# Optimization experiments

Hardware: AMD Instinct MI355X
Metric: run time of the kernel (lower is better)

The kernel has to match this reference:

```python
import jax, jax.numpy as jnp
import numpy as np
from jax import lax

N = 2; C_IN = 256
H0, W0 = 100, 152
H1, W1 = 50, 76
DYN_CH = 34            # 4 init_offset + 4 bound_pt_offset + 18 semantic_pt_offset + 8 reg_aggr_attn
REG_CH = 4             # 4 boundary points x 1 channel each
NUM_CLASSES = 80
SEM_PTS = 9
CLS_CH = SEM_PTS * NUM_CLASSES
BOUND_PTS = 4
RATIO = 0.5            # LIMIT_BOUND_POINT_OFFSET_RATIO

_BASE = np.array([[1,0,0,0],[0,1,0,0],[0.5,0,0.5,0],
                  [0,0.5,0,0.5],[0,0,1,0],[0,0,0,1]], np.float32)
BOUND_MAT = jnp.asarray(_BASE[[0,3,2,1,4,3,2,5]])                      # (8,4) box -> cross-shaped 4 pts
SEM_MAT = jnp.asarray(_BASE[[0,1,0,3,0,5,2,1,2,3,2,5,4,1,4,3,4,5]])    # (18,4) box -> 3x3 pts
BOUND_OFF_IDX = jnp.array([1, 2, 5, 6])   # tangential coordinate channel of each boundary point
LOC_IDX = jnp.array([0, 3, 4, 7])         # box-side coordinate channel of each boundary point

def conv3x3(x, w, b):
    y = lax.conv_general_dilated(x, w, (1, 1), 'SAME',
                                 dimension_numbers=('NCHW', 'OIHW', 'NCHW'))
    return y + b[None, :, None, None]

def conv1x1(x, w):
    return jnp.einsum('oi,nihw->nohw', w[:, :, 0, 0], x)

def pred_collect(fmap, pts, point_num, reduce_points, bias=None):
    # Bilinearly sample per-point channel groups of fmap at dynamic point locations.
    # fmap: (N, P*c, Hm, Wm); pts: (N, 2P, H, W) with (x, y) pairs per point.
    Nb, C, Hm, Wm = fmap.shape
    P = point_num; c = C // P
    H, W = pts.shape[2], pts.shape[3]
    fm = fmap.reshape(Nb, P, c, Hm, Wm)
    pg = pts.reshape(Nb, P, 2, H, W)
    def sample(f, pt):  # f: (c, Hm, Wm), pt: (2, H, W)
        x = jnp.clip(pt[0], 0.0, Wm - 1.0)
        y = jnp.clip(pt[1], 0.0, Hm - 1.0)
        x0 = jnp.floor(x); y0 = jnp.floor(y)
        fx = x - x0; fy = y - y0
        x0i = x0.astype(jnp.int32); y0i = y0.astype(jnp.int32)
        x1i = jnp.minimum(x0i + 1, Wm - 1); y1i = jnp.minimum(y0i + 1, Hm - 1)
        v00 = f[:, y0i, x0i]; v01 = f[:, y0i, x1i]
        v10 = f[:, y1i, x0i]; v11 = f[:, y1i, x1i]
        return v00*(1-fx)*(1-fy) + v01*fx*(1-fy) + v10*(1-fx)*fy + v11*fx*fy
    vals = jax.vmap(jax.vmap(sample))(fm, pg)  # (N, P, c, H, W)
    if reduce_points:
        out = vals.sum(axis=1)
        if bias is not None:
            out = out + bias[None, :, None, None]
        return out
    return vals.reshape(Nb, P * c, H, W)

def head_forward(reg_feats, cls_feats, anchors, dyn_w, dyn_b, reg_w, cls_w, cls_b):
    reg_maps = [conv1x1(x, reg_w) for x in reg_feats]
    cls_maps = [conv1x1(x, cls_w) for x in cls_feats]
    cls_scores, coarse_boxes, reg_boxes = [], [], []
    for i, (reg_feat, anchor) in enumerate(zip(reg_feats, anchors)):
        Nb, _, H, W = reg_feat.shape
        pred = conv3x3(reg_feat, dyn_w, dyn_b)
        init_off, bpt_off, spt_off, attn = jnp.split(pred, [4, 8, 26], axis=1)
        coarse = anchor + init_off                                  # (N,4,H,W) = (x1,y1,x2,y2)
        # straight-through clamp of boundary-point tangential offsets to +-wh/2*ratio
        bpt_off = bpt_off.reshape(Nb, 2, 2, 1, H, W)
        wh = jnp.stack([coarse[:, 3] - coarse[:, 1],
                        coarse[:, 2] - coarse[:, 0]], axis=1) / 2 * RATIO  # (N,2,H,W) [h,w]
        thres = wh[:, None, :, None]                                # (N,1,2,1,H,W)
        extra = jnp.maximum(bpt_off - thres, 0.0) + jnp.minimum(bpt_off + thres, 0.0)
        bpt_off = (bpt_off - lax.stop_gradient(extra)).reshape(Nb, 4, H, W)
        bound_pt = lax.stop_gradient(jnp.einsum('oc,nchw->nohw', BOUND_MAT, coarse))
        bound_pt = bound_pt.at[:, BOUND_OFF_IDX].add(bpt_off)       # (N,8,H,W)
        bound_pt_loc = bound_pt[:, LOC_IDX]                         # (N,4,H,W)
        reg_val = pred_collect(reg_maps[i], bound_pt, BOUND_PTS, False)  # (N,4,H,W)
        if i > 0:
            attn_sm = jax.nn.softmax(attn.reshape(Nb, BOUND_PTS, 2, H, W), axis=2)
            reg_hi = reg_val.reshape(Nb, BOUND_PTS, 1, 1, H, W)
            reg_lo = pred_collect(reg_maps[i - 1], bound_pt * 2, BOUND_PTS, False)
            reg_lo = reg_lo.reshape(Nb, BOUND_PTS, 1, 1, H, W) * 0.5
            reg_val = (jnp.concatenate([reg_lo, reg_hi], axis=2)
                       * attn_sm[:, :, :, None]).sum(axis=2).reshape(Nb, -1, H, W)
        reg_box = (lax.stop_gradient(bound_pt_loc) + reg_val).reshape(Nb, 4, -1, H, W).mean(axis=2)
        sem_pt = lax.stop_gradient(jnp.einsum('oc,nchw->nohw', SEM_MAT, coarse)) + spt_off
        cls_score = pred_collect(cls_maps[i], sem_pt, SEM_PTS, True, cls_b)  # (N,80,H,W)
        cls_scores.append(cls_score); coarse_boxes.append(coarse); reg_boxes.append(reg_box)
    return cls_scores, coarse_boxes, reg_boxes

def make_anchor(H, W):
    gy, gx = jnp.meshgrid(jnp.arange(H, dtype=jnp.float32),
                          jnp.arange(W, dtype=jnp.float32), indexing='ij')
    a = jnp.stack([gx - 4.0, gy - 4.0, gx + 4.0, gy + 4.0], axis=0)
    return jnp.broadcast_to(a[None], (N, 4, H, W))

def setup_inputs() -> dict:
    key = jax.random.key(0)
    ks = jax.random.split(key, 7)
    return {
        "reg_feat0": jax.random.normal(ks[0], (N, C_IN, H0, W0), jnp.float32),
        "reg_feat1": jax.random.normal(ks[1], (N, C_IN, H1, W1), jnp.float32),
        "cls_feat0": jax.random.normal(ks[2], (N, C_IN, H0, W0), jnp.float32),
        "cls_feat1": jax.random.normal(ks[3], (N, C_IN, H1, W1), jnp.float32),
        "anchor0": make_anchor(H0, W0),
        "anchor1": make_anchor(H1, W1),
        "dyn_w": jax.random.normal(ks[4], (DYN_CH, C_IN, 3, 3), jnp.float32) * 0.01,
        "dyn_b": jnp.zeros((DYN_CH,), jnp.float32),
        "reg_w": jax.random.normal(ks[5], (REG_CH, C_IN, 1, 1), jnp.float32) * 0.05,
        "cls_w": jax.random.normal(ks[6], (CLS_CH, C_IN, 1, 1), jnp.float32) * 0.05,
        "cls_b": jnp.zeros((NUM_CLASSES,), jnp.float32),
    }

def reference(reg_feat0, reg_feat1, cls_feat0, cls_feat1, anchor0, anchor1,
              dyn_w, dyn_b, reg_w, cls_w, cls_b):
    cls_scores, coarse_boxes, reg_boxes = head_forward(
        [reg_feat0, reg_feat1], [cls_feat0, cls_feat1], [anchor0, anchor1],
        dyn_w, dyn_b, reg_w, cls_w, cls_b)
    return (*cls_scores, *coarse_boxes, *reg_boxes)
```

## Files before the change

### kernel.cpp

```cpp
#include <hip/hip_runtime.h>
#include <hip/hip_bf16.h>
#include <cstdint>

#define N_BATCH 2
#define C_IN 256
#define DYN_CH 34
#define CLS_CH 720
#define NUM_CLASSES 80
#define NCOMB 48

#define P0c 15200
#define P1c 3800
#define M0c 30400
#define M1c 7600
#define MT0c 119
#define MT1c 30
#define CT0c 475
#define CT1c 119

typedef __attribute__((ext_vector_type(8))) short short8;
typedef __attribute__((ext_vector_type(4))) float f32x4;

typedef const unsigned int __attribute__((address_space(1)))* gas1_t;
typedef unsigned int __attribute__((address_space(3)))* las3_t;

__device__ __forceinline__ void async_ld16(const void* g, void* l) {
  __builtin_amdgcn_global_load_lds((gas1_t)g, (las3_t)l, 16, 0, 0);
}

__global__ __launch_bounds__(256) void pack_feat(
    const float* __restrict__ cls0, const float* __restrict__ cls1,
    const float* __restrict__ reg0, const float* __restrict__ reg1,
    const float* __restrict__ cls_w, const float* __restrict__ dyn_w,
    const float* __restrict__ reg_w, __hip_bfloat16* __restrict__ a0,
    __hip_bfloat16* __restrict__ a1, __hip_bfloat16* __restrict__ r0,
    __hip_bfloat16* __restrict__ r1, __hip_bfloat16* __restrict__ bpack,
    __hip_bfloat16* __restrict__ wpack) {
  int b = blockIdx.x;
  if (b >= 2384) {
    b -= 2384;
    if (b < 90) {
      int u = b * 256 + threadIdx.x;
      if (u >= 9 * 32 * 80) return;
      int ntile = u / 2560;
      int rem = u % 2560;
      int kcg = rem / 80;
      int ochl = rem % 80;
      int och = ntile * 80 + ochl;
      const float* wr = cls_w + (size_t)och * C_IN + kcg * 8;
      __hip_bfloat16 tmp[8];
#pragma unroll
      for (int c = 0; c < 8; ++c) tmp[c] = __float2bfloat16(wr[c]);
      *(uint4*)(bpack + (size_t)u * 8) = *(const uint4*)tmp;
    } else {
      int u = (b - 90) * 256 + threadIdx.x;
      if (u >= 13824) return;
      int j = u / 768;
      int r = u % 768;
      int n = r / 16;
      int s = r % 16;
      int ku = j * 16 + (s ^ (n & 7));
      int k0 = ku * 8;
      int tap = k0 >> 8;
      int c0 = k0 & 255;
      __hip_bfloat16 tmp[8];
#pragma unroll
      for (int i = 0; i < 8; ++i) {
        int c = c0 + i;
        float v = 0.f;
        if (n < DYN_CH) v = dyn_w[((size_t)n * C_IN + c) * 9 + tap];
        else if (n < DYN_CH + 4 && tap == 4)
          v = reg_w[(size_t)(n - DYN_CH) * C_IN + c];
        tmp[i] = __float2bfloat16(v);
      }
      *(uint4*)(wpack + (size_t)u * 8) = *(const uint4*)tmp;
    }
    return;
  }
  int j = b & 7;
  int mtg = b >> 3;
  const float* src;
  __hip_bfloat16* dst;
  int P, Mtot, mtile;
  if (mtg < 119)      { src = cls0; dst = a0; P = P0c; Mtot = M0c; mtile = mtg; }
  else if (mtg < 149) { src = cls1; dst = a1; P = P1c; Mtot = M1c; mtile = mtg - 119; }
  else if (mtg < 268) { src = reg0; dst = r0; P = P0c; Mtot = M0c; mtile = mtg - 149; }
  else                { src = reg1; dst = r1; P = P1c; Mtot = M1c; mtile = mtg - 268; }
  int wave = threadIdx.x >> 6;
  int lane = threadIdx.x & 63;
  int kcg = j * 4 + wave;
  int c0 = kcg * 8;
  int m4 = mtile * 256 + lane * 4;
  uint4* du = (uint4*)dst + (size_t)mtile * 8192 + (size_t)kcg * 256 + lane * 4;
  if (m4 < Mtot) {
    int n = m4 / P;
    int p = m4 - n * P;
    const float* sp = src + ((size_t)n * C_IN + c0) * P + p;
    float4 f[8];
#pragma unroll
    for (int c = 0; c < 8; ++c) f[c] = *(const float4*)(sp + (size_t)c * P);
#pragma unroll
    for (int i = 0; i < 4; ++i) {
      union { uint4 u; __hip_bfloat16 h[8]; } o;
#pragma unroll
      for (int c = 0; c < 8; ++c) {
        float v = (i == 0) ? f[c].x : (i == 1) ? f[c].y : (i == 2) ? f[c].z : f[c].w;
        o.h[c] = __float2bfloat16(v);
      }
      du[i] = o.u;
    }
  } else {
    uint4 z = {0u, 0u, 0u, 0u};
#pragma unroll
    for (int i = 0; i < 4; ++i) du[i] = z;
  }
}

__global__ __launch_bounds__(512) void cls_gemm_mfma(
    const uint4* __restrict__ Ap0, const uint4* __restrict__ Ap1,
    const uint4* __restrict__ Bp, __hip_bfloat16* __restrict__ out0,
    __hip_bfloat16* __restrict__ out1) {
  __shared__ uint4 Bsh[2560];
  int bb = blockIdx.x;
  int g = bb & 7;
  int loc = bb >> 3;
  int lm = loc / 9;
  int ntile = loc - lm * 9;
  int mtile = g * 19 + lm;
  if (mtile >= MT0c + MT1c) return;
  int tid = threadIdx.x;
  int w = tid >> 6;
  int lane = tid & 63;
  int l15 = lane & 15;
  int kq = lane >> 4;

  const uint4* Ap;
  __hip_bfloat16* out;
  int Mtot;
  if (mtile < MT0c) { Ap = Ap0; out = out0; Mtot = M0c; }
  else              { mtile -= MT0c; Ap = Ap1; out = out1; Mtot = M1c; }

  const uint4* Ab = Ap + (size_t)mtile * 8192;
  const uint4* Bb = Bp + (size_t)ntile * 2560;

#pragma unroll
  for (int i = 0; i < 5; ++i)
    async_ld16(Bb + i * 512 + w * 64 + lane, &Bsh[i * 512 + w * 64]);
  __syncthreads();

  f32x4 acc[2][5];
#pragma unroll
  for (int i = 0; i < 2; ++i)
#pragma unroll
    for (int j = 0; j < 5; ++j) acc[i][j] = (f32x4)0.f;

  const uint4* Abase = Ab + kq * 256 + w * 32 + l15;
#pragma unroll 2
  for (int kb = 0; kb < 8; ++kb) {
    uint4 a[2];
#pragma unroll
    for (int mi = 0; mi < 2; ++mi) a[mi] = Abase[kb * 1024 + mi * 16];
    short8 b[5];
    const uint4* Br = &Bsh[kb * 320 + kq * 80 + l15];
#pragma unroll
    for (int ni = 0; ni < 5; ++ni) b[ni] = *(const short8*)&Br[ni * 16];
#pragma unroll
    for (int mi = 0; mi < 2; ++mi)
#pragma unroll
      for (int ni = 0; ni < 5; ++ni)
        acc[mi][ni] = __builtin_amdgcn_mfma_f32_16x16x32_bf16(
            *(const short8*)&a[mi], b[ni], acc[mi][ni], 0, 0, 0);
  }

  int gbase = mtile * 256 + w * 32;
#pragma unroll
  for (int mi = 0; mi < 2; ++mi) {
#pragma unroll
    for (int r = 0; r < 4; ++r) {
      int gg = gbase + mi * 16 + kq * 4 + r;
      if (gg >= Mtot) continue;
      __hip_bfloat16* orow = out + (size_t)gg * CLS_CH + ntile * 80 + l15;
#pragma unroll
      for (int ni = 0; ni < 5; ++ni)
        orow[ni * 16] = __float2bfloat16(acc[mi][ni][r]);
    }
  }
}

__global__ __launch_bounds__(256) void dyn_reg_conv_mfma(
    const uint4* __restrict__ rp0, const uint4* __restrict__ rp1,
    const uint4* __restrict__ wp, float* __restrict__ part0,
    float* __restrict__ part1) {
  __shared__ uint4 Bs[768];
  int g = blockIdx.x & 7;
  int loc = blockIdx.x >> 3;
  int lm = loc / 3;
  int seg = loc - lm * 3;
  int bx = g * 75 + lm;
  if (bx >= CT0c + CT1c) return;
  int tid = threadIdx.x;
  int wave = tid >> 6;
  int lane = tid & 63;
  int l15 = lane & 15;
  int kq = lane >> 4;

  const uint4* rp;
  float* part;
  int Mtot, P, W, H;
  if (bx < CT0c) { rp = rp0; part = part0; Mtot = M0c; P = P0c; W = 152; H = 100; }
  else { bx -= CT0c; rp = rp1; part = part1; Mtot = M1c; P = P1c; W = 76; H = 50; }

  int m = bx * 64 + wave * 16 + l15;
  bool mval = (m < Mtot);
  int mc = mval ? m : 0;
  int n = mc / P;
  int rem = mc - n * P;
  int y = rem / W;
  int x = rem - y * W;

  f32x4 acc[3];
#pragma unroll
  for (int i = 0; i < 3; ++i) acc[i] = (f32x4)0.f;

  for (int jj = 0; jj < 6; ++jj) {
    int j = seg * 6 + jj;
    const uint4* wsrc = wp + (size_t)j * 768 + wave * 192;
#pragma unroll
    for (int i = 0; i < 3; ++i)
      async_ld16(wsrc + i * 64 + lane, &Bs[wave * 192 + i * 64]);

    int tap = j >> 1;
    int cb8 = (j & 1) * 16;
    int dy = tap / 3 - 1, dx = tap % 3 - 1;
    int sy = y + dy, sx = x + dx;
    bool val = mval && ((unsigned)sy < (unsigned)H) && ((unsigned)sx < (unsigned)W);
    int sm = m + dy * W + dx;
    int smc = val ? sm : 0;
    size_t tbase = (size_t)(smc >> 8) * 8192 + (smc & 255);
    uint4 a[4];
#pragma unroll
    for (int t = 0; t < 4; ++t) {
      uint4 v = {0u, 0u, 0u, 0u};
      if (val) v = rp[tbase + (size_t)(cb8 + t * 4 + kq) * 256];
      a[t] = v;
    }
    __syncthreads();
#pragma unroll
    for (int t = 0; t < 4; ++t) {
#pragma unroll
      for (int ni = 0; ni < 3; ++ni) {
        int nn = ni * 16 + l15;
        short8 bf = *(const short8*)&Bs[nn * 16 + ((t * 4 + kq) ^ (nn & 7))];
        acc[ni] = __builtin_amdgcn_mfma_f32_16x16x32_bf16(
            *(short8*)&a[t], bf, acc[ni], 0, 0, 0);
      }
    }
    __syncthreads();
  }

  int mrow = bx * 64 + wave * 16 + kq * 4;
#pragma unroll
  for (int r = 0; r < 4; ++r) {
    int mm = mrow + r;
    if (mm >= Mtot) continue;
    float* dst = part + ((size_t)seg * Mtot + mm) * NCOMB + l15;
#pragma unroll
    for (int ni = 0; ni < 3; ++ni) dst[ni * 16] = acc[ni][r];
  }
}

__device__ __forceinline__ float samp48(const float* __restrict__ part,
                                        int Mtot, int nbase, int W, int H,
                                        float px, float py, int ch) {
  float xc = fminf(fmaxf(px, 0.f), (float)(W - 1));
  float yc = fminf(fmaxf(py, 0.f), (float)(H - 1));
  float x0f = floorf(xc), y0f = floorf(yc);
  float fx = xc - x0f, fy = yc - y0f;
  int x0 = (int)x0f, y0 = (int)y0f;
  int x1 = min(x0 + 1, W - 1), y1 = min(y0 + 1, H - 1);
  size_t m00 = (size_t)(nbase + y0 * W + x0);
  size_t m01 = (size_t)(nbase + y0 * W + x1);
  size_t m10 = (size_t)(nbase + y1 * W + x0);
  size_t m11 = (size_t)(nbase + y1 * W + x1);
  float v00 = 0.f, v01 = 0.f, v10 = 0.f, v11 = 0.f;
#pragma unroll
  for (int s = 0; s < 3; ++s) {
    size_t off = (size_t)s * Mtot;
    v00 += part[(off + m00) * NCOMB + ch];
    v01 += part[(off + m01) * NCOMB + ch];
    v10 += part[(off + m10) * NCOMB + ch];
    v11 += part[(off + m11) * NCOMB + ch];
  }
  return v00 * (1.f - fx) * (1.f - fy) + v01 * fx * (1.f - fy) +
         v10 * (1.f - fx) * fy + v11 * fx * fy;
}

__global__ __launch_bounds__(64) void decode(
    const float* __restrict__ part0, const float* __restrict__ part1,
    const float* __restrict__ dyn_b, const float* __restrict__ anchor0,
    const float* __restrict__ anchor1, float* __restrict__ out_coarse0,
    float* __restrict__ out_coarse1, float* __restrict__ out_regbox0,
    float* __restrict__ out_regbox1, int4* __restrict__ sidx0,
    float4* __restrict__ swt0, int4* __restrict__ sidx1,
    float4* __restrict__ swt1) {
  int g = blockIdx.x & 7;
  int loc = blockIdx.x >> 3;
  int u = g * 75 + loc;
  if (u >= 594) return;
  const float* part;
  const float* anchor;
  float* out_coarse;
  float* out_regbox;
  int4* sidx;
  float4* swt;
  int Mtot, H, W, P, level, m;
  if (u < 475) {
    part = part0; anchor = anchor0; out_coarse = out_coarse0;
    out_regbox = out_regbox0; sidx = sidx0; swt = swt0;
    Mtot = M0c; H = 100; W = 152; P = P0c; level = 0;
    m = u * 64 + threadIdx.x;
  } else {
    part = part1; anchor = anchor1; out_coarse = out_coarse1;
    out_regbox = out_regbox1; sidx = sidx1; swt = swt1;
    Mtot = M1c; H = 50; W = 76; P = P1c; level = 1;
    m = (u - 475) * 64 + threadIdx.x;
  }
  if (m >= Mtot) return;
  int n = m / P;
  int p = m - n * P;
  float pr[40];
  {
    const float4* q0 = (const float4*)(part + (size_t)m * NCOMB);
    const float4* q1 = (const float4*)(part + ((size_t)Mtot + m) * NCOMB);
    const float4* q2 = (const float4*)(part + ((size_t)2 * Mtot + m) * NCOMB);
#pragma unroll
    for (int o4 = 0; o4 < 10; ++o4) {
      float4 a = q0[o4], b = q1[o4], c = q2[o4];
      pr[4 * o4 + 0] = a.x + b.x + c.x;
      pr[4 * o4 + 1] = a.y + b.y + c.y;
      pr[4 * o4 + 2] = a.z + b.z + c.z;
      pr[4 * o4 + 3] = a.w + b.w + c.w;
    }
#pragma unroll
    for (int o = 0; o < DYN_CH; ++o) pr[o] += dyn_b[o];
  }
  const float* an = anchor + (size_t)n * 4 * P + p;
  float cb[4];
#pragma unroll
  for (int k = 0; k < 4; ++k) cb[k] = an[(size_t)k * P] + pr[k];
  float* oc = out_coarse + (size_t)n * 4 * P + p;
#pragma unroll
  for (int k = 0; k < 4; ++k) oc[(size_t)k * P] = cb[k];

  float thr_y = (cb[3] - cb[1]) * 0.25f;
  float thr_x = (cb[2] - cb[0]) * 0.25f;
  float bo[4];
#pragma unroll
  for (int j = 0; j < 4; ++j) {
    float thr = (j & 1) ? thr_x : thr_y;
    float b = pr[4 + j];
    float extra = fmaxf(b - thr, 0.f) + fminf(b + thr, 0.f);
    bo[j] = b - extra;
  }
  float cx = 0.5f * (cb[0] + cb[2]);
  float cy = 0.5f * (cb[1] + cb[3]);
  float bp[8] = {cb[0], cy + bo[0], cx + bo[1], cb[1],
                 cb[2], cy + bo[2], cx + bo[3], cb[3]};

  int nbase = n * P;
  int nbaseLo = n * P0c;
  float rb[4];
#pragma unroll
  for (int pt = 0; pt < 4; ++pt) {
    float hi = samp48(part, Mtot, nbase, W, H, bp[2 * pt], bp[2 * pt + 1],
                      DYN_CH + pt);
    float val;
    if (level == 0) {
      val = hi;
    } else {
      float lo = 0.5f * samp48(part0, M0c, nbaseLo, 152, 100, bp[2 * pt] * 2.f,
                               bp[2 * pt + 1] * 2.f, DYN_CH + pt);
      float e0 = pr[26 + 2 * pt], e1 = pr[26 + 2 * pt + 1];
      float mx = fmaxf(e0, e1);
      float w0 = expf(e0 - mx), w1 = expf(e1 - mx);
      val = (lo * w0 + hi * w1) / (w0 + w1);
    }
    rb[pt] = val;
  }
  float* orb = out_regbox + (size_t)n * 4 * P + p;
  orb[0] = bp[0] + rb[0];
  orb[(size_t)P] = bp[3] + rb[1];
  orb[(size_t)2 * P] = bp[4] + rb[2];
  orb[(size_t)3 * P] = bp[7] + rb[3];

  float sx[9] = {cb[0], cb[0], cb[0], cx, cx, cx, cb[2], cb[2], cb[2]};
  float sy[9] = {cb[1], cy, cb[3], cb[1], cy, cb[3], cb[1], cy, cb[3]};
#pragma unroll
  for (int k = 0; k < 9; ++k) {
    float px = sx[k] + pr[8 + 2 * k];
    float py = sy[k] + pr[8 + 2 * k + 1];
    float xc = fminf(fmaxf(px, 0.f), (float)(W - 1));
    float yc = fminf(fmaxf(py, 0.f), (float)(H - 1));
    float x0f = floorf(xc), y0f = floorf(yc);
    float fx = xc - x0f, fy = yc - y0f;
    int x0 = (int)x0f, y0 = (int)y0f;
    int x1 = min(x0 + 1, W - 1), y1 = min(y0 + 1, H - 1);
    int4 iv;
    iv.x = (nbase + y0 * W + x0) * CLS_CH + k * 80;
    iv.y = (x1 - x0) * CLS_CH;
    iv.z = (y1 - y0) * W * CLS_CH;
    iv.w = 0;
    sidx[(size_t)k * Mtot + m] = iv;
    float4 wv = {(1.f - fx) * (1.f - fy), fx * (1.f - fy), (1.f - fx) * fy,
                 fx * fy};
    swt[(size_t)k * Mtot + m] = wv;
  }
}

__global__ __launch_bounds__(256) void cls_gather_f(
    const __hip_bfloat16* __restrict__ map0,
    const __hip_bfloat16* __restrict__ map1, const int4* __restrict__ sidx0,
    const float4* __restrict__ swt0, const int4* __restrict__ sidx1,
    const float4* __restrict__ swt1, const float* __restrict__ bias,
    float* __restrict__ outc0, float* __restrict__ outc1) {
  __shared__ float lds[NUM_CLASSES * 5];
  int b = (blockIdx.x & 7) * 1188 + (blockIdx.x >> 3);
  if (b >= 9500) return;
  const __hip_bfloat16* map;
  const int4* sidx;
  const float4* swt;
  float* out;
  int Mtot, P;
  if (b < 7600) { map = map0; sidx = sidx0; swt = swt0; out = outc0; Mtot = M0c; P = P0c; }
  else { b -= 7600; map = map1; sidx = sidx1; swt = swt1; out = outc1; Mtot = M1c; P = P1c; }
  int lane = threadIdx.x & 63;
  int wv = threadIdx.x >> 6;
  int m = b * 4 + wv;

  int sub = lane / 20;
  if (sub > 2) sub = 2;
  int cl = lane % 20;
  int c4 = cl * 4;

  float a0 = 0.f, a1 = 0.f, a2 = 0.f, a3 = 0.f;
#pragma unroll
  for (int g = 0; g < 3; ++g) {
    int pt = g * 3 + sub;
    int4 iv = sidx[(size_t)pt * Mtot + m];
    float4 wt = swt[(size_t)pt * Mtot + m];
    const __hip_bfloat16* pl = map + iv.x + c4;
    uint2 t00 = *(const uint2*)(pl);
    uint2 t01 = *(const uint2*)(pl + iv.y);
    uint2 t10 = *(const uint2*)(pl + iv.z);
    uint2 t11 = *(const uint2*)(pl + iv.y + iv.z);
    a0 += wt.x * __uint_as_float(t00.x << 16) +
          wt.y * __uint_as_float(t01.x << 16) +
          wt.z * __uint_as_float(t10.x << 16) +
          wt.w * __uint_as_float(t11.x << 16);
    a1 += wt.x * __uint_as_float(t00.x & 0xffff0000u) +
          wt.y * __uint_as_float(t01.x & 0xffff0000u) +
          wt.z * __uint_as_float(t10.x & 0xffff0000u) +
          wt.w * __uint_as_float(t11.x & 0xffff0000u);
    a2 += wt.x * __uint_as_float(t00.y << 16) +
          wt.y * __uint_as_float(t01.y << 16) +
          wt.z * __uint_as_float(t10.y << 16) +
          wt.w * __uint_as_float(t11.y << 16);
    a3 += wt.x * __uint_as_float(t00.y & 0xffff0000u) +
          wt.y * __uint_as_float(t01.y & 0xffff0000u) +
          wt.z * __uint_as_float(t10.y & 0xffff0000u) +
          wt.w * __uint_as_float(t11.y & 0xffff0000u);
  }
  {
    float s0 = __shfl(a0, lane + 20), u0 = __shfl(a0, lane + 40);
    float s1 = __shfl(a1, lane + 20), u1 = __shfl(a1, lane + 40);
    float s2 = __shfl(a2, lane + 20), u2 = __shfl(a2, lane + 40);
    float s3 = __shfl(a3, lane + 20), u3 = __shfl(a3, lane + 40);
    a0 += s0 + u0;
    a1 += s1 + u1;
    a2 += s2 + u2;
    a3 += s3 + u3;
  }
  if (lane < 20) {
    lds[(c4 + 0) * 5 + wv] = a0;
    lds[(c4 + 1) * 5 + wv] = a1;
    lds[(c4 + 2) * 5 + wv] = a2;
    lds[(c4 + 3) * 5 + wv] = a3;
  }
  __syncthreads();
  int tid = threadIdx.x;
  if (tid < NUM_CLASSES) {
    float bb = bias[tid];
    float4 v = {lds[tid * 5] + bb, lds[tid * 5 + 1] + bb, lds[tid * 5 + 2] + bb,
                lds[tid * 5 + 3] + bb};
    int m0 = b * 4;
    int n = m0 / P;
    int p0 = m0 - n * P;
    *(float4*)&out[((size_t)n * NUM_CLASSES + tid) * P + p0] = v;
  }
}

extern "C" void kernel_launch(void* const* d_in, const int* in_sizes, int n_in,
                              void* d_out, int out_size, void* d_ws,
                              size_t ws_size, hipStream_t stream) {
  const float* reg_feat0 = (const float*)d_in[0];
  const float* reg_feat1 = (const float*)d_in[1];
  const float* cls_feat0 = (const float*)d_in[2];
  const float* cls_feat1 = (const float*)d_in[3];
  const float* anchor0 = (const float*)d_in[4];
  const float* anchor1 = (const float*)d_in[5];
  const float* dyn_w = (const float*)d_in[6];
  const float* dyn_b = (const float*)d_in[7];
  const float* reg_w = (const float*)d_in[8];
  const float* cls_w = (const float*)d_in[9];
  const float* cls_b = (const float*)d_in[10];

  float* out = (float*)d_out;
  float* out_cls0 = out;
  float* out_cls1 = out_cls0 + (size_t)N_BATCH * NUM_CLASSES * P0c;
  float* out_coarse0 = out_cls1 + (size_t)N_BATCH * NUM_CLASSES * P1c;
  float* out_coarse1 = out_coarse0 + (size_t)N_BATCH * 4 * P0c;
  float* out_reg0 = out_coarse1 + (size_t)N_BATCH * 4 * P1c;
  float* out_reg1 = out_reg0 + (size_t)N_BATCH * 4 * P0c;

  char* w = (char*)d_ws;
  __hip_bfloat16* bpack = (__hip_bfloat16*)w;   w += 368640;
  __hip_bfloat16* wpack = (__hip_bfloat16*)w;   w += 221184;
  char* apack_base = w;
  __hip_bfloat16* apack0 = (__hip_bfloat16*)w;  w += 15597568;
  __hip_bfloat16* apack1 = (__hip_bfloat16*)w;  w += 3932160;
  char* rpack_base = w;
  __hip_bfloat16* rpack0 = (__hip_bfloat16*)w;  w += 15597568;
  __hip_bfloat16* rpack1 = (__hip_bfloat16*)w;  w += 3932160;
  float* part1 = (float*)w;                     w += 4377600;
  __hip_bfloat16* map0 = (__hip_bfloat16*)w;    w += 43776000;
  __hip_bfloat16* map1 = (__hip_bfloat16*)w;    w += 10944000;
  float* part0 = (float*)apack_base;
  int4* sidx0 = (int4*)rpack_base;
  float4* swt0 = (float4*)(rpack_base + 4377600);
  int4* sidx1 = (int4*)(rpack_base + 8755200);
  float4* swt1 = (float4*)(rpack_base + 9849600);

  hipLaunchKernelGGL(pack_feat, dim3(2528), dim3(256), 0, stream, cls_feat0,
                     cls_feat1, reg_feat0, reg_feat1, cls_w, dyn_w, reg_w,
                     apack0, apack1, rpack0, rpack1, bpack, wpack);
  hipLaunchKernelGGL(cls_gemm_mfma, dim3(8 * 19 * 9), dim3(512), 0, stream,
                     (const uint4*)apack0, (const uint4*)apack1,
                     (const uint4*)bpack, map0, map1);
  hipLaunchKernelGGL(dyn_reg_conv_mfma, dim3(1800), dim3(256), 0,
                     stream, (const uint4*)rpack0, (const uint4*)rpack1,
                     (const uint4*)wpack, part0, part1);
  hipLaunchKernelGGL(decode, dim3(600), dim3(64), 0, stream, part0,
                     part1, dyn_b, anchor0, anchor1, out_coarse0, out_coarse1,
                     out_reg0, out_reg1, sidx0, swt0, sidx1, swt1);
  hipLaunchKernelGGL(cls_gather_f, dim3(9504), dim3(256), 0, stream, map0,
                     map1, sidx0, swt0, sidx1, swt1, cls_b, out_cls0, out_cls1);
}
```

Before: 223.1 us.

## Fuse cls GEMM and dynamic conv into one launch with block-range dispatch

Merges the cls 1x1 GEMM kernel and the dynamic 3x3 conv kernel into a single launch. Blocks below a fixed index run the GEMM; the remaining blocks run the conv, each 512-thread block now covering two 64-row conv tiles and sharing the weight tile in LDS. This lets the two independent workloads overlap on the GPU and removes one launch plus the tail gap between them. Because the GEMM's A-pack buffer is still being read while the conv writes its partial sums, part0 gets its own workspace region instead of aliasing that buffer, which costs extra workspace memory.

```diff
diff --git a/kernel.cpp b/kernel.cpp
--- a/kernel.cpp
+++ b/kernel.cpp
@@ -116,101 +116,102 @@
   }
 }
 
-__global__ __launch_bounds__(512) void cls_gemm_mfma(
+__global__ __launch_bounds__(512) void gemm_conv_fused(
     const uint4* __restrict__ Ap0, const uint4* __restrict__ Ap1,
     const uint4* __restrict__ Bp, __hip_bfloat16* __restrict__ out0,
-    __hip_bfloat16* __restrict__ out1) {
-  __shared__ uint4 Bsh[2560];
-  int bb = blockIdx.x;
-  int g = bb & 7;
-  int loc = bb >> 3;
-  int lm = loc / 9;
-  int ntile = loc - lm * 9;
-  int mtile = g * 19 + lm;
-  if (mtile >= MT0c + MT1c) return;
-  int tid = threadIdx.x;
-  int w = tid >> 6;
-  int lane = tid & 63;
-  int l15 = lane & 15;
-  int kq = lane >> 4;
-
-  const uint4* Ap;
-  __hip_bfloat16* out;
-  int Mtot;
-  if (mtile < MT0c) { Ap = Ap0; out = out0; Mtot = M0c; }
-  else              { mtile -= MT0c; Ap = Ap1; out = out1; Mtot = M1c; }
-
-  const uint4* Ab = Ap + (size_t)mtile * 8192;
-  const uint4* Bb = Bp + (size_t)ntile * 2560;
-
-#pragma unroll
-  for (int i = 0; i < 5; ++i)
-    async_ld16(Bb + i * 512 + w * 64 + lane, &Bsh[i * 512 + w * 64]);
-  __syncthreads();
-
-  f32x4 acc[2][5];
-#pragma unroll
-  for (int i = 0; i < 2; ++i)
-#pragma unroll
-    for (int j = 0; j < 5; ++j) acc[i][j] = (f32x4)0.f;
-
-  const uint4* Abase = Ab + kq * 256 + w * 32 + l15;
-#pragma unroll 2
-  for (int kb = 0; kb < 8; ++kb) {
-    uint4 a[2];
-#pragma unroll
-    for (int mi = 0; mi < 2; ++mi) a[mi] = Abase[kb * 1024 + mi * 16];
-    short8 b[5];
-    const uint4* Br = &Bsh[kb * 320 + kq * 80 + l15];
-#pragma unroll
-    for (int ni = 0; ni < 5; ++ni) b[ni] = *(const short8*)&Br[ni * 16];
-#pragma unroll
-    for (int mi = 0; mi < 2; ++mi)
-#pragma unroll
-      for (int ni = 0; ni < 5; ++ni)
-        acc[mi][ni] = __builtin_amdgcn_mfma_f32_16x16x32_bf16(
-            *(const short8*)&a[mi], b[ni], acc[mi][ni], 0, 0, 0);
-  }
-
-  int gbase = mtile * 256 + w * 32;
-#pragma unroll
-  for (int mi = 0; mi < 2; ++mi) {
-#pragma unroll
-    for (int r = 0; r < 4; ++r) {
-      int gg = gbase + mi * 16 + kq * 4 + r;
-      if (gg >= Mtot) continue;
-      __hip_bfloat16* orow = out + (size_t)gg * CLS_CH + ntile * 80 + l15;
-#pragma unroll
-      for (int ni = 0; ni < 5; ++ni)
-        orow[ni * 16] = __float2bfloat16(acc[mi][ni][r]);
-    }
-  }
-}
-
-__global__ __launch_bounds__(256) void dyn_reg_conv_mfma(
-    const uint4* __restrict__ rp0, const uint4* __restrict__ rp1,
-    const uint4* __restrict__ wp, float* __restrict__ part0,
-    float* __restrict__ part1) {
-  __shared__ uint4 Bs[768];
-  int g = blockIdx.x & 7;
-  int loc = blockIdx.x >> 3;
-  int lm = loc / 3;
-  int seg = loc - lm * 3;
-  int bx = g * 75 + lm;
-  if (bx >= CT0c + CT1c) return;
+    __hip_bfloat16* __restrict__ out1, const uint4* __restrict__ rp0,
+    const uint4* __restrict__ rp1, const uint4* __restrict__ wp,
+    float* __restrict__ part0, float* __restrict__ part1) {
+  __shared__ uint4 sh[2560];
   int tid = threadIdx.x;
   int wave = tid >> 6;
   int lane = tid & 63;
   int l15 = lane & 15;
   int kq = lane >> 4;
 
+  if (blockIdx.x < 1368) {
+    int bb = blockIdx.x;
+    int g = bb & 7;
+    int loc = bb >> 3;
+    int lm = loc / 9;
+    int ntile = loc - lm * 9;
+    int mtile = g * 19 + lm;
+    if (mtile >= MT0c + MT1c) return;
+
+    const uint4* Ap;
+    __hip_bfloat16* out;
+    int Mtot;
+    if (mtile < MT0c) { Ap = Ap0; out = out0; Mtot = M0c; }
+    else              { mtile -= MT0c; Ap = Ap1; out = out1; Mtot = M1c; }
+
+    const uint4* Ab = Ap + (size_t)mtile * 8192;
+    const uint4* Bb = Bp + (size_t)ntile * 2560;
+
+#pragma unroll
+    for (int i = 0; i < 5; ++i)
+      async_ld16(Bb + i * 512 + wave * 64 + lane, &sh[i * 512 + wave * 64]);
+    __syncthreads();
+
+    f32x4 acc[2][5];
+#pragma unroll
+    for (int i = 0; i < 2; ++i)
+#pragma unroll
+      for (int j = 0; j < 5; ++j) acc[i][j] = (f32x4)0.f;
+
+    const uint4* Abase = Ab + kq * 256 + wave * 32 + l15;
+#pragma unroll 2
+    for (int kb = 0; kb < 8; ++kb) {
+      uint4 a[2];
+#pragma unroll
+      for (int mi = 0; mi < 2; ++mi) a[mi] = Abase[kb * 1024 + mi * 16];
+      short8 b[5];
+      const uint4* Br = &sh[kb * 320 + kq * 80 + l15];
+#pragma unroll
+      for (int ni = 0; ni < 5; ++ni) b[ni] = *(const short8*)&Br[ni * 16];
+#pragma unroll
+      for (int mi = 0; mi < 2; ++mi)
+#pragma unroll
+        for (int ni = 0; ni < 5; ++ni)
+          acc[mi][ni] = __builtin_amdgcn_mfma_f32_16x16x32_bf16(
+              *(const short8*)&a[mi], b[ni], acc[mi][ni], 0, 0, 0);
+    }
+
+    int gbase = mtile * 256 + wave * 32;
+#pragma unroll
+    for (int mi = 0; mi < 2; ++mi) {
+#pragma unroll
+      for (int r = 0; r < 4; ++r) {
+        int gg = gbase + mi * 16 + kq * 4 + r;
+        if (gg >= Mtot) continue;
+        __hip_bfloat16* orow = out + (size_t)gg * CLS_CH + ntile * 80 + l15;
+#pragma unroll
+        for (int ni = 0; ni < 5; ++ni)
+          orow[ni * 16] = __float2bfloat16(acc[mi][ni][r]);
+      }
+    }
+    return;
+  }
+
+  int c = blockIdx.x - 1368;
+  int g = c & 7;
+  int i = c >> 3;
+  int cnt = (g < 3) ? 112 : 111;
+  if (i >= cnt) return;
+  int start = g * 111 + (g < 3 ? g : 3);
+  int wuu = start + i;
+  int t = wuu / 3;
+  int seg = wuu - t * 3;
+  int half = wave >> 2;
+  int lw = wave & 3;
+  int bx = t * 2 + half;
+
   const uint4* rp;
   float* part;
   int Mtot, P, W, H;
   if (bx < CT0c) { rp = rp0; part = part0; Mtot = M0c; P = P0c; W = 152; H = 100; }
   else { bx -= CT0c; rp = rp1; part = part1; Mtot = M1c; P = P1c; W = 76; H = 50; }
 
-  int m = bx * 64 + wave * 16 + l15;
+  int m = bx * 64 + lw * 16 + l15;
   bool mval = (m < Mtot);
   int mc = mval ? m : 0;
   int n = mc / P;
@@ -220,14 +221,16 @@
 
   f32x4 acc[3];
 #pragma unroll
-  for (int i = 0; i < 3; ++i) acc[i] = (f32x4)0.f;
+  for (int q = 0; q < 3; ++q) acc[q] = (f32x4)0.f;
 
   for (int jj = 0; jj < 6; ++jj) {
     int j = seg * 6 + jj;
-    const uint4* wsrc = wp + (size_t)j * 768 + wave * 192;
-#pragma unroll
-    for (int i = 0; i < 3; ++i)
-      async_ld16(wsrc + i * 64 + lane, &Bs[wave * 192 + i * 64]);
+    if (wave < 4) {
+      const uint4* wsrc = wp + (size_t)j * 768 + wave * 192;
+#pragma unroll
+      for (int q = 0; q < 3; ++q)
+        async_ld16(wsrc + q * 64 + lane, &sh[wave * 192 + q * 64]);
+    }
 
     int tap = j >> 1;
     int cb8 = (j & 1) * 16;
@@ -239,26 +242,26 @@
     size_t tbase = (size_t)(smc >> 8) * 8192 + (smc & 255);
     uint4 a[4];
 #pragma unroll
-    for (int t = 0; t < 4; ++t) {
+    for (int tt = 0; tt < 4; ++tt) {
       uint4 v = {0u, 0u, 0u, 0u};
-      if (val) v = rp[tbase + (size_t)(cb8 + t * 4 + kq) * 256];
-      a[t] = v;
+      if (val) v = rp[tbase + (size_t)(cb8 + tt * 4 + kq) * 256];
+      a[tt] = v;
     }
     __syncthreads();
 #pragma unroll
-    for (int t = 0; t < 4; ++t) {
+    for (int tt = 0; tt < 4; ++tt) {
 #pragma unroll
       for (int ni = 0; ni < 3; ++ni) {
         int nn = ni * 16 + l15;
-        short8 bf = *(const short8*)&Bs[nn * 16 + ((t * 4 + kq) ^ (nn & 7))];
+        short8 bf = *(const short8*)&sh[nn * 16 + ((tt * 4 + kq) ^ (nn & 7))];
         acc[ni] = __builtin_amdgcn_mfma_f32_16x16x32_bf16(
-            *(short8*)&a[t], bf, acc[ni], 0, 0, 0);
+            *(short8*)&a[tt], bf, acc[ni], 0, 0, 0);
       }
     }
     __syncthreads();
   }
 
-  int mrow = bx * 64 + wave * 16 + kq * 4;
+  int mrow = bx * 64 + lw * 16 + kq * 4;
 #pragma unroll
   for (int r = 0; r < 4; ++r) {
     int mm = mrow + r;
@@ -525,7 +528,6 @@
   char* w = (char*)d_ws;
   __hip_bfloat16* bpack = (__hip_bfloat16*)w;   w += 368640;
   __hip_bfloat16* wpack = (__hip_bfloat16*)w;   w += 221184;
-  char* apack_base = w;
   __hip_bfloat16* apack0 = (__hip_bfloat16*)w;  w += 15597568;
   __hip_bfloat16* apack1 = (__hip_bfloat16*)w;  w += 3932160;
   char* rpack_base = w;
@@ -534,7 +536,7 @@
   float* part1 = (float*)w;                     w += 4377600;
   __hip_bfloat16* map0 = (__hip_bfloat16*)w;    w += 43776000;
   __hip_bfloat16* map1 = (__hip_bfloat16*)w;    w += 10944000;
-  float* part0 = (float*)apack_base;
+  float* part0 = (float*)w;                     w += 17510400;
   int4* sidx0 = (int4*)rpack_base;
   float4* swt0 = (float4*)(rpack_base + 4377600);
   int4* sidx1 = (int4*)(rpack_base + 8755200);
@@ -543,12 +545,10 @@
   hipLaunchKernelGGL(pack_feat, dim3(2528), dim3(256), 0, stream, cls_feat0,
                      cls_feat1, reg_feat0, reg_feat1, cls_w, dyn_w, reg_w,
                      apack0, apack1, rpack0, rpack1, bpack, wpack);
-  hipLaunchKernelGGL(cls_gemm_mfma, dim3(8 * 19 * 9), dim3(512), 0, stream,
+  hipLaunchKernelGGL(gemm_conv_fused, dim3(2264), dim3(512), 0, stream,
                      (const uint4*)apack0, (const uint4*)apack1,
-                     (const uint4*)bpack, map0, map1);
-  hipLaunchKernelGGL(dyn_reg_conv_mfma, dim3(1800), dim3(256), 0,
-                     stream, (const uint4*)rpack0, (const uint4*)rpack1,
-                     (const uint4*)wpack, part0, part1);
+                     (const uint4*)bpack, map0, map1, (const uint4*)rpack0,
+                     (const uint4*)rpack1, (const uint4*)wpack, part0, part1);
   hipLaunchKernelGGL(decode, dim3(600), dim3(64), 0, stream, part0,
                      part1, dyn_b, anchor0, anchor1, out_coarse0, out_coarse1,
                      out_reg0, out_reg1, sidx0, swt0, sidx1, swt1);
```

After: 227.0 us. Within noise of the previous version (+1.7%).
